# Kernel optimization log

Hardware: AMD Instinct MI355X
Metric: run time of the kernel (lower is better)

## Reference

```python
import jax, jax.numpy as jnp
import numpy as np

N = 100000      # nodes
E = 3200000     # edges (before self-loops)
F_IN = 512      # input feature dim
H1, H2 = 64, 128
C = 40          # num classes
EPS = 1e-5      # BatchNorm eps


def setup_inputs() -> dict:
    key = jax.random.key(0)
    ks = jax.random.split(key, 20)
    inp = {
        "x": jax.random.normal(ks[0], (N, F_IN), jnp.float32),
        "edge_index": jax.random.randint(ks[1], (2, E), 0, N, dtype=jnp.int64),
        # GCNConv weights/biases (glorot-ish scale)
        "W1": jax.random.normal(ks[2], (F_IN, H1), jnp.float32) * (1.0 / np.sqrt(F_IN)),
        "b1": jnp.zeros((H1,), jnp.float32),
        "W2": jax.random.normal(ks[3], (H1, H2), jnp.float32) * (1.0 / np.sqrt(H1)),
        "b2": jnp.zeros((H2,), jnp.float32),
        "W3": jax.random.normal(ks[4], (H2, C), jnp.float32) * (1.0 / np.sqrt(H2)),
        "b3": jnp.zeros((C,), jnp.float32),
        # BatchNorm (eval mode: running stats)
        "g1": 1.0 + 0.1 * jax.random.normal(ks[5], (H1,), jnp.float32),
        "bt1": 0.1 * jax.random.normal(ks[6], (H1,), jnp.float32),
        "rm1": 0.1 * jax.random.normal(ks[7], (H1,), jnp.float32),
        "rv1": jax.random.uniform(ks[8], (H1,), jnp.float32, 0.5, 1.5),
        "g2": 1.0 + 0.1 * jax.random.normal(ks[9], (H2,), jnp.float32),
        "bt2": 0.1 * jax.random.normal(ks[10], (H2,), jnp.float32),
        "rm2": 0.1 * jax.random.normal(ks[11], (H2,), jnp.float32),
        "rv2": jax.random.uniform(ks[12], (H2,), jnp.float32, 0.5, 1.5),
    }
    return inp


def _gcn_norm(edge_index):
    # add self-loops, compute sym-normalized edge weights: d^-1/2[src]*d^-1/2[dst]
    loop = jnp.arange(N, dtype=edge_index.dtype)
    src = jnp.concatenate([edge_index[0], loop])
    dst = jnp.concatenate([edge_index[1], loop])
    deg = jax.ops.segment_sum(jnp.ones_like(dst, jnp.float32), dst, num_segments=N)
    dinv = 1.0 / jnp.sqrt(deg)  # deg >= 1 thanks to self-loops
    norm = dinv[src] * dinv[dst]  # [E+N]
    return src, dst, norm


def _gcn_conv(x, W, b, src, dst, norm):
    h = x @ W                                   # [N, out]
    msg = h[src] * norm[:, None]                # [E+N, out] gather + per-edge scale
    agg = jax.ops.segment_sum(msg, dst, num_segments=N)  # scatter-add
    return agg + b


def _bn_eval(x, gamma, beta, mean, var):
    return (x - mean) * (gamma / jnp.sqrt(var + EPS)) + beta


def reference(x, edge_index, W1, b1, W2, b2, W3, b3,
              g1, bt1, rm1, rv1, g2, bt2, rm2, rv2):
    src, dst, norm = _gcn_norm(edge_index)
    h = jax.nn.relu(_bn_eval(_gcn_conv(x, W1, b1, src, dst, norm), g1, bt1, rm1, rv1))
    # dropout p=0.3: identity in eval mode
    h = jax.nn.relu(_bn_eval(_gcn_conv(h, W2, b2, src, dst, norm), g2, bt2, rm2, rv2))
    h = _gcn_conv(h, W3, b3, src, dst, norm)
    return jax.nn.log_softmax(h, axis=1)
```

## Files before the change

### kernel.cpp

```cpp
#include <hip/hip_runtime.h>
#include <hip/hip_bf16.h>

#define NN 100000
#define FIN 512
#define H1D 64
#define H2D 128
#define CD 40
#define GP 64
#define BNEPS 1e-5f

#define BSHIFT 9
#define BSZ 512
#define NB 196
#define CHUNK 8192

typedef __attribute__((ext_vector_type(8))) short bf16x8;
typedef __attribute__((ext_vector_type(4))) float f32x4;

__device__ __forceinline__ float bf2f(ushort u) {
    union { uint i; float f; } v; v.i = ((uint)u) << 16; return v.f;
}
__device__ __forceinline__ ushort f2bf(float f) {
    union { float f; uint i; } v; v.f = f;
    uint x = v.i;
    return (ushort)((x + 0x7fffu + ((x >> 16) & 1u)) >> 16);
}

__device__ __forceinline__ void acc8(float* a, uint4 v) {
    a[0] += bf2f((ushort)(v.x & 0xffff)); a[1] += bf2f((ushort)(v.x >> 16));
    a[2] += bf2f((ushort)(v.y & 0xffff)); a[3] += bf2f((ushort)(v.y >> 16));
    a[4] += bf2f((ushort)(v.z & 0xffff)); a[5] += bf2f((ushort)(v.z >> 16));
    a[6] += bf2f((ushort)(v.w & 0xffff)); a[7] += bf2f((ushort)(v.w >> 16));
}


__global__ __launch_bounds__(256) void bhist_k(const int* __restrict__ dst, int E,
                                               int* __restrict__ bcount) {
    __shared__ int h[NB];
    for (int i = threadIdx.x; i < NB; i += 256) h[i] = 0;
    __syncthreads();
    int i = blockIdx.x * blockDim.x + threadIdx.x;
    int st = gridDim.x * blockDim.x;
    for (; i < E; i += st) atomicAdd(&h[dst[i] >> BSHIFT], 1);
    __syncthreads();
    for (int j = threadIdx.x; j < NB; j += 256)
        if (h[j]) atomicAdd(&bcount[j], h[j]);
}

__global__ __launch_bounds__(256) void bscan_k(const int* __restrict__ bcount,
                                               int* __restrict__ bstart,
                                               int* __restrict__ bcursor) {
    __shared__ int sh[NB];
    int tid = threadIdx.x;
    if (tid < NB) sh[tid] = bcount[tid];
    __syncthreads();
    for (int off = 1; off < NB; off <<= 1) {
        int v = (tid < NB && tid >= off) ? sh[tid - off] : 0;
        __syncthreads();
        if (tid < NB) sh[tid] += v;
        __syncthreads();
    }
    if (tid < NB) {
        int s = tid ? sh[tid - 1] : 0;
        bstart[tid] = s;
        bcursor[tid] = s;
    }
    if (tid == 0) bstart[NB] = sh[NB - 1];
}

__global__ __launch_bounds__(256) void bscatter_k(const int* __restrict__ src,
                                                  const int* __restrict__ dst, int E,
                                                  int* __restrict__ bcursor,
                                                  int* __restrict__ ebuf) {
    __shared__ int hist[NB];
    __shared__ int loff[NB];
    __shared__ int lcur[NB];
    __shared__ int gbase[NB];
    __shared__ int sbuf[CHUNK];
    int tid = threadIdx.x;
    int e0 = blockIdx.x * CHUNK;
    int e1 = e0 + CHUNK; if (e1 > E) e1 = E;

    for (int i = tid; i < NB; i += 256) hist[i] = 0;
    __syncthreads();
    for (int i = e0 + tid; i < e1; i += 256) atomicAdd(&hist[dst[i] >> BSHIFT], 1);
    __syncthreads();
    int v = (tid < NB) ? hist[tid] : 0;
    __syncthreads();
    if (tid < NB) loff[tid] = v;
    __syncthreads();
    for (int off = 1; off < NB; off <<= 1) {
        int u = (tid < NB && tid >= off) ? loff[tid - off] : 0;
        __syncthreads();
        if (tid < NB) loff[tid] += u;
        __syncthreads();
    }
    if (tid < NB) {
        int excl = loff[tid] - v;
        loff[tid] = excl;
        lcur[tid] = excl;
        gbase[tid] = (v > 0) ? atomicAdd(&bcursor[tid], v) : 0;
    }
    __syncthreads();
    for (int i = e0 + tid; i < e1; i += 256) {
        int d = dst[i];
        int b = d >> BSHIFT;
        int pos = atomicAdd(&lcur[b], 1);
        sbuf[pos] = (src[i] << BSHIFT) | (d & (BSZ - 1));
    }
    __syncthreads();
    int wave = tid >> 6, lane = tid & 63;
    for (int b = wave; b < NB; b += 4) {
        int cnt = (b + 1 < NB ? loff[b + 1] : (e1 - e0)) - loff[b];
        int s0 = loff[b], d0 = gbase[b];
        for (int k = lane; k < cnt; k += 64) ebuf[d0 + k] = sbuf[s0 + k];
    }
}

__global__ __launch_bounds__(256) void bcsr_k(const int* __restrict__ ebuf,
                                              const int* __restrict__ bstart,
                                              int* __restrict__ rowstart,
                                              float* __restrict__ dinv,
                                              int* __restrict__ csr, int E) {
    __shared__ int ldeg[BSZ];
    __shared__ int lcur[BSZ];
    __shared__ int s2[256];
    int b = blockIdx.x, tid = threadIdx.x;
    int node0 = b << BSHIFT;
    int es = bstart[b], ee = bstart[b + 1];
    ldeg[tid] = 0; ldeg[tid + 256] = 0;
    __syncthreads();
    for (int i = es + tid; i < ee; i += 256) atomicAdd(&ldeg[ebuf[i] & (BSZ - 1)], 1);
    __syncthreads();
    int a0 = ldeg[2 * tid], a1 = ldeg[2 * tid + 1];
    s2[tid] = a0 + a1;
    __syncthreads();
    for (int off = 1; off < 256; off <<= 1) {
        int u = (tid >= off) ? s2[tid - off] : 0;
        __syncthreads();
        s2[tid] += u;
        __syncthreads();
    }
    int base2 = tid ? s2[tid - 1] : 0;
    int ex0 = base2, ex1 = base2 + a0;
    int n0 = node0 + 2 * tid, n1 = n0 + 1;
    if (n0 < NN) { rowstart[n0] = es + ex0; dinv[n0] = rsqrtf((float)(a0 + 1)); }
    if (n1 < NN) { rowstart[n1] = es + ex1; dinv[n1] = rsqrtf((float)(a1 + 1)); }
    lcur[2 * tid] = es + ex0;
    lcur[2 * tid + 1] = es + ex1;
    __syncthreads();
    for (int i = es + tid; i < ee; i += 256) {
        int e = ebuf[i];
        int pos = atomicAdd(&lcur[e & (BSZ - 1)], 1);
        csr[pos] = ((unsigned)e) >> BSHIFT;
    }
    if (b == 0 && tid == 0) rowstart[NN] = E;
}

__global__ __launch_bounds__(256) void w1cvt_k(const float* __restrict__ W1,
                                               ushort* __restrict__ w1t) {
    int i = blockIdx.x * 256 + threadIdx.x;
    if (i < FIN * H1D) {
        int n = i >> 9, k = i & 511;
        w1t[i] = f2bf(W1[k * H1D + n]);
    }
}

#define BPAD 520
__global__ __launch_bounds__(256) void gemm1_k(const float* __restrict__ x,
                                               const ushort* __restrict__ w1t,
                                               const float* __restrict__ dinv,
                                               ushort* __restrict__ t1) {
    __shared__ ushort sB[H1D * BPAD];
    int tid = threadIdx.x;
    {
        int row = tid >> 2, seg = tid & 3;
        const uint4* srcp = (const uint4*)(w1t + row * FIN + seg * 128);
        uint4* dstp = (uint4*)(sB + row * BPAD + seg * 128);
#pragma unroll
        for (int j = 0; j < 16; ++j) dstp[j] = srcp[j];
    }
    __syncthreads();
    int wave = tid >> 6, lane = tid & 63;
    int lm = lane & 15, q = lane >> 4;
    int r0 = blockIdx.x * 64 + wave * 16;
    int mrow = r0 + lm;
    int mc = mrow < NN ? mrow : NN - 1;
    const float* ap = x + (size_t)mc * FIN + q * 8;
    const ushort* bp = sB + (size_t)lm * BPAD + q * 8;
    f32x4 acc0 = {0.f, 0.f, 0.f, 0.f}, acc1 = acc0, acc2 = acc0, acc3 = acc0;
#pragma unroll 4
    for (int kb = 0; kb < FIN; kb += 32) {
        float4 a01 = *(const float4*)(ap + kb);
        float4 a23 = *(const float4*)(ap + kb + 4);
        union { bf16x8 v8; __hip_bfloat162 h2[4]; } ua;
        ua.h2[0] = __float22bfloat162_rn(make_float2(a01.x, a01.y));
        ua.h2[1] = __float22bfloat162_rn(make_float2(a01.z, a01.w));
        ua.h2[2] = __float22bfloat162_rn(make_float2(a23.x, a23.y));
        ua.h2[3] = __float22bfloat162_rn(make_float2(a23.z, a23.w));
        bf16x8 b0 = *(const bf16x8*)(bp + kb);
        bf16x8 b1 = *(const bf16x8*)(bp + 16 * BPAD + kb);
        bf16x8 b2 = *(const bf16x8*)(bp + 32 * BPAD + kb);
        bf16x8 b3 = *(const bf16x8*)(bp + 48 * BPAD + kb);
        acc0 = __builtin_amdgcn_mfma_f32_16x16x32_bf16(ua.v8, b0, acc0, 0, 0, 0);
        acc1 = __builtin_amdgcn_mfma_f32_16x16x32_bf16(ua.v8, b1, acc1, 0, 0, 0);
        acc2 = __builtin_amdgcn_mfma_f32_16x16x32_bf16(ua.v8, b2, acc2, 0, 0, 0);
        acc3 = __builtin_amdgcn_mfma_f32_16x16x32_bf16(ua.v8, b3, acc3, 0, 0, 0);
    }
    int rbase = r0 + q * 4;
#pragma unroll
    for (int r = 0; r < 4; ++r) {
        int row = rbase + r;
        if (row < NN) {
            float dv = dinv[row];
            ushort* o = t1 + (size_t)row * H1D;
            o[lm]      = f2bf(acc0[r] * dv);
            o[16 + lm] = f2bf(acc1[r] * dv);
            o[32 + lm] = f2bf(acc2[r] * dv);
            o[48 + lm] = f2bf(acc3[r] * dv);
        }
    }
}

template <int MODE>
__global__ __launch_bounds__(256) void agg64_k(const ushort* __restrict__ tin,
                                               ushort* __restrict__ tout,
                                               const int* __restrict__ rowstart,
                                               const int* __restrict__ csr,
                                               const float* __restrict__ dinv,
                                               const float* __restrict__ g,
                                               const float* __restrict__ bt,
                                               const float* __restrict__ rm,
                                               const float* __restrict__ rv,
                                               const float* __restrict__ b) {
    int wid = (blockIdx.x * blockDim.x + threadIdx.x) >> 6;
    int lane = threadIdx.x & 63;
    if (wid >= NN) return;
    int gsl = lane >> 3;
    int c   = lane & 7;
    int rs = rowstart[wid], re = rowstart[wid + 1];
    float a[8];
#pragma unroll
    for (int j = 0; j < 8; ++j) a[j] = 0.f;
    int i = rs;
    for (; i + 32 <= re; i += 32) {
        int s0 = csr[i + gsl];
        int s1 = csr[i + 8 + gsl];
        int s2 = csr[i + 16 + gsl];
        int s3 = csr[i + 24 + gsl];
        uint4 v0 = *(const uint4*)(tin + (size_t)s0 * H1D + 8 * c);
        uint4 v1 = *(const uint4*)(tin + (size_t)s1 * H1D + 8 * c);
        uint4 v2 = *(const uint4*)(tin + (size_t)s2 * H1D + 8 * c);
        uint4 v3 = *(const uint4*)(tin + (size_t)s3 * H1D + 8 * c);
        acc8(a, v0); acc8(a, v1); acc8(a, v2); acc8(a, v3);
    }
    for (; i + 8 <= re; i += 8) {
        int s0 = csr[i + gsl];
        uint4 v0 = *(const uint4*)(tin + (size_t)s0 * H1D + 8 * c);
        acc8(a, v0);
    }
    if (i + gsl < re) {
        int s0 = csr[i + gsl];
        uint4 v0 = *(const uint4*)(tin + (size_t)s0 * H1D + 8 * c);
        acc8(a, v0);
    }
#pragma unroll
    for (int j = 0; j < 8; ++j) a[j] += __shfl_xor(a[j], 8);
#pragma unroll
    for (int j = 0; j < 8; ++j) a[j] += __shfl_xor(a[j], 16);
#pragma unroll
    for (int j = 0; j < 8; ++j) a[j] += __shfl_xor(a[j], 32);
    {
        uint4 sv = *(const uint4*)(tin + (size_t)wid * H1D + 8 * c);
        acc8(a, sv);
    }
    float dv = dinv[wid];
    float z[8];
    if (MODE == 1) {
        int f0 = 8 * c;
        float4 G0 = *(const float4*)(g + f0),  G1 = *(const float4*)(g + f0 + 4);
        float4 V0 = *(const float4*)(rv + f0), V1 = *(const float4*)(rv + f0 + 4);
        float4 B0 = *(const float4*)(b + f0),  B1 = *(const float4*)(b + f0 + 4);
        float4 M0 = *(const float4*)(rm + f0), M1 = *(const float4*)(rm + f0 + 4);
        float4 T0 = *(const float4*)(bt + f0), T1 = *(const float4*)(bt + f0 + 4);
        float sc[8] = { G0.x * rsqrtf(V0.x + BNEPS), G0.y * rsqrtf(V0.y + BNEPS),
                        G0.z * rsqrtf(V0.z + BNEPS), G0.w * rsqrtf(V0.w + BNEPS),
                        G1.x * rsqrtf(V1.x + BNEPS), G1.y * rsqrtf(V1.y + BNEPS),
                        G1.z * rsqrtf(V1.z + BNEPS), G1.w * rsqrtf(V1.w + BNEPS) };
        float sh[8] = { (B0.x - M0.x) * sc[0] + T0.x, (B0.y - M0.y) * sc[1] + T0.y,
                        (B0.z - M0.z) * sc[2] + T0.z, (B0.w - M0.w) * sc[3] + T0.w,
                        (B1.x - M1.x) * sc[4] + T1.x, (B1.y - M1.y) * sc[5] + T1.y,
                        (B1.z - M1.z) * sc[6] + T1.z, (B1.w - M1.w) * sc[7] + T1.w };
#pragma unroll
        for (int j = 0; j < 8; ++j)
            z[j] = fmaxf(a[j] * dv * sc[j] + sh[j], 0.f) * dv;
    } else {
#pragma unroll
        for (int j = 0; j < 8; ++j) z[j] = a[j] * dv;
    }
    if (gsl == 0) {
        uint4 o;
        o.x = (uint)f2bf(z[0]) | ((uint)f2bf(z[1]) << 16);
        o.y = (uint)f2bf(z[2]) | ((uint)f2bf(z[3]) << 16);
        o.z = (uint)f2bf(z[4]) | ((uint)f2bf(z[5]) << 16);
        o.w = (uint)f2bf(z[6]) | ((uint)f2bf(z[7]) << 16);
        *(uint4*)(tout + (size_t)wid * H1D + 8 * c) = o;
    }
}

__global__ __launch_bounds__(256) void p2p3_k(const ushort* __restrict__ u2,
                                              const float* __restrict__ W2,
                                              const float* __restrict__ b2,
                                              const float* __restrict__ W3,
                                              const float* __restrict__ g2,
                                              const float* __restrict__ bt2,
                                              const float* __restrict__ rm2,
                                              const float* __restrict__ rv2,
                                              const float* __restrict__ dinv,
                                              ushort* __restrict__ g3) {
    __shared__ float sW2[H1D * H2D];
    __shared__ float sW3[H2D * CD];
    __shared__ float sc2[H2D], sh2[H2D];
    int tid = threadIdx.x;
    for (int i = tid; i < H1D * H2D; i += 256) sW2[i] = W2[i];
    for (int i = tid; i < H2D * CD; i += 256) sW3[i] = W3[i];
    if (tid < H2D) {
        float s = g2[tid] * rsqrtf(rv2[tid] + BNEPS);
        sc2[tid] = s;
        sh2[tid] = (b2[tid] - rm2[tid]) * s + bt2[tid];
    }
    __syncthreads();
    int node = blockIdx.x * 256 + tid;
    if (node >= NN) return;
    float u[H1D];
    const uint4* up = (const uint4*)(u2 + (size_t)node * H1D);
#pragma unroll
    for (int i = 0; i < 8; ++i) {
        uint4 v = up[i];
        u[8 * i + 0] = bf2f((ushort)(v.x & 0xffff)); u[8 * i + 1] = bf2f((ushort)(v.x >> 16));
        u[8 * i + 2] = bf2f((ushort)(v.y & 0xffff)); u[8 * i + 3] = bf2f((ushort)(v.y >> 16));
        u[8 * i + 4] = bf2f((ushort)(v.z & 0xffff)); u[8 * i + 5] = bf2f((ushort)(v.z >> 16));
        u[8 * i + 6] = bf2f((ushort)(v.w & 0xffff)); u[8 * i + 7] = bf2f((ushort)(v.w >> 16));
    }
    float gacc[CD];
#pragma unroll
    for (int c = 0; c < CD; ++c) gacc[c] = 0.f;
    for (int fc = 0; fc < H2D; fc += 32) {
        float a[32];
#pragma unroll
        for (int j = 0; j < 32; ++j) a[j] = 0.f;
        for (int l = 0; l < H1D; ++l) {
            float ul = u[l];
            const float4* wr = (const float4*)&sW2[l * H2D + fc];
#pragma unroll
            for (int j = 0; j < 8; ++j) {
                float4 w = wr[j];
                a[4 * j]     += ul * w.x;
                a[4 * j + 1] += ul * w.y;
                a[4 * j + 2] += ul * w.z;
                a[4 * j + 3] += ul * w.w;
            }
        }
#pragma unroll
        for (int j = 0; j < 32; ++j) {
            int f = fc + j;
            float hv = fmaxf(a[j] * sc2[f] + sh2[f], 0.f);
            const float4* w3r = (const float4*)&sW3[f * CD];
#pragma unroll
            for (int c = 0; c < 10; ++c) {
                float4 w = w3r[c];
                gacc[4 * c]     += hv * w.x;
                gacc[4 * c + 1] += hv * w.y;
                gacc[4 * c + 2] += hv * w.z;
                gacc[4 * c + 3] += hv * w.w;
            }
        }
    }
    float dv = dinv[node];
    ushort* op = g3 + (size_t)node * GP;
#pragma unroll
    for (int c = 0; c < 10; ++c) {
        uint pk  = (uint)f2bf(gacc[4 * c] * dv)     | ((uint)f2bf(gacc[4 * c + 1] * dv) << 16);
        uint pk2 = (uint)f2bf(gacc[4 * c + 2] * dv) | ((uint)f2bf(gacc[4 * c + 3] * dv) << 16);
        *(uint2*)&op[4 * c] = make_uint2(pk, pk2);
    }
}

__global__ __launch_bounds__(256) void agg40_k(const ushort* __restrict__ g3,
                                               const float* __restrict__ b3,
                                               const int* __restrict__ rowstart,
                                               const int* __restrict__ csr,
                                               const float* __restrict__ dinv,
                                               float* __restrict__ out) {
    int wid = (blockIdx.x * blockDim.x + threadIdx.x) >> 6;
    int lane = threadIdx.x & 63;
    if (wid >= NN) return;
    int gsl = lane >> 3;
    int c   = lane & 7;
    int rs = rowstart[wid], re = rowstart[wid + 1];
    float a[8];
#pragma unroll
    for (int j = 0; j < 8; ++j) a[j] = 0.f;
    if (c < 5) {
        int i = rs;
        for (; i + 32 <= re; i += 32) {
            int s0 = csr[i + gsl];
            int s1 = csr[i + 8 + gsl];
            int s2 = csr[i + 16 + gsl];
            int s3 = csr[i + 24 + gsl];
            uint4 v0 = *(const uint4*)(g3 + (size_t)s0 * GP + 8 * c);
            uint4 v1 = *(const uint4*)(g3 + (size_t)s1 * GP + 8 * c);
            uint4 v2 = *(const uint4*)(g3 + (size_t)s2 * GP + 8 * c);
            uint4 v3 = *(const uint4*)(g3 + (size_t)s3 * GP + 8 * c);
            acc8(a, v0); acc8(a, v1); acc8(a, v2); acc8(a, v3);
        }
        for (; i + 8 <= re; i += 8) {
            int s0 = csr[i + gsl];
            uint4 v0 = *(const uint4*)(g3 + (size_t)s0 * GP + 8 * c);
            acc8(a, v0);
        }
        if (i + gsl < re) {
            int s0 = csr[i + gsl];
            uint4 v0 = *(const uint4*)(g3 + (size_t)s0 * GP + 8 * c);
            acc8(a, v0);
        }
    }
#pragma unroll
    for (int j = 0; j < 8; ++j) a[j] += __shfl_xor(a[j], 8);
#pragma unroll
    for (int j = 0; j < 8; ++j) a[j] += __shfl_xor(a[j], 16);
#pragma unroll
    for (int j = 0; j < 8; ++j) a[j] += __shfl_xor(a[j], 32);
    if (c < 5) {
        uint4 sv = *(const uint4*)(g3 + (size_t)wid * GP + 8 * c);
        acc8(a, sv);
    }
    float dv = dinv[wid];
    float z[8];
    if (c < 5) {
        int f0 = 8 * c;
        float4 bb0 = *(const float4*)(b3 + f0);
        float4 bb1 = *(const float4*)(b3 + f0 + 4);
        z[0] = a[0] * dv + bb0.x; z[1] = a[1] * dv + bb0.y;
        z[2] = a[2] * dv + bb0.z; z[3] = a[3] * dv + bb0.w;
        z[4] = a[4] * dv + bb1.x; z[5] = a[5] * dv + bb1.y;
        z[6] = a[6] * dv + bb1.z; z[7] = a[7] * dv + bb1.w;
    } else {
#pragma unroll
        for (int j = 0; j < 8; ++j) z[j] = -1e30f;
    }
    float m = fmaxf(fmaxf(fmaxf(z[0], z[1]), fmaxf(z[2], z[3])),
                    fmaxf(fmaxf(z[4], z[5]), fmaxf(z[6], z[7])));
    m = fmaxf(m, __shfl_xor(m, 1));
    m = fmaxf(m, __shfl_xor(m, 2));
    m = fmaxf(m, __shfl_xor(m, 4));
    float e = 0.f;
    if (c < 5) {
#pragma unroll
        for (int j = 0; j < 8; ++j) e += __expf(z[j] - m);
    }
    e += __shfl_xor(e, 1);
    e += __shfl_xor(e, 2);
    e += __shfl_xor(e, 4);
    float ls = __logf(e);
    if (gsl == 0 && c < 5) {
        int f0 = 8 * c;
        float4 o0 = { z[0] - m - ls, z[1] - m - ls, z[2] - m - ls, z[3] - m - ls };
        float4 o1 = { z[4] - m - ls, z[5] - m - ls, z[6] - m - ls, z[7] - m - ls };
        *(float4*)(out + (size_t)wid * CD + f0)     = o0;
        *(float4*)(out + (size_t)wid * CD + f0 + 4) = o1;
    }
}


extern "C" void kernel_launch(void* const* d_in, const int* in_sizes, int n_in,
                              void* d_out, int out_size, void* d_ws, size_t ws_size,
                              hipStream_t stream) {
    (void)n_in; (void)out_size; (void)ws_size;
    const float* x   = (const float*)d_in[0];
    const int*   ei  = (const int*)d_in[1];
    const float* W1  = (const float*)d_in[2];
    const float* b1  = (const float*)d_in[3];
    const float* W2  = (const float*)d_in[4];
    const float* b2  = (const float*)d_in[5];
    const float* W3  = (const float*)d_in[6];
    const float* b3  = (const float*)d_in[7];
    const float* g1  = (const float*)d_in[8];
    const float* bt1 = (const float*)d_in[9];
    const float* rm1 = (const float*)d_in[10];
    const float* rv1 = (const float*)d_in[11];
    const float* g2  = (const float*)d_in[12];
    const float* bt2 = (const float*)d_in[13];
    const float* rm2 = (const float*)d_in[14];
    const float* rv2 = (const float*)d_in[15];
    float* out = (float*)d_out;
    const int E = in_sizes[1] / 2;

    char* w = (char*)d_ws;
    auto alloc = [&](size_t bytes) { char* p = w; w += (bytes + 511) & ~(size_t)511; return p; };
    int*    bcount   = (int*)alloc((size_t)NB * 4);
    int*    bstart   = (int*)alloc((size_t)(NB + 1) * 4);
    int*    bcursor  = (int*)alloc((size_t)NB * 4);
    int*    rowstart = (int*)alloc((size_t)(NN + 1) * 4);
    float*  dinv     = (float*)alloc((size_t)NN * 4);
    int*    csr      = (int*)alloc((size_t)E * 4);
    int*    ebuf     = (int*)alloc((size_t)E * 4);
    ushort* w1t      = (ushort*)alloc((size_t)H1D * FIN * 2);
    ushort* t1       = (ushort*)alloc((size_t)NN * H1D * 2);
    ushort* t2       = (ushort*)alloc((size_t)NN * H1D * 2);
    ushort* g3       = (ushort*)alloc((size_t)NN * GP * 2);

    hipMemsetAsync(bcount, 0, (size_t)NB * 4, stream);
    bhist_k<<<512, 256, 0, stream>>>(ei + E, E, bcount);
    bscan_k<<<1, 256, 0, stream>>>(bcount, bstart, bcursor);
    bscatter_k<<<(E + CHUNK - 1) / CHUNK, 256, 0, stream>>>(ei, ei + E, E, bcursor, ebuf);
    bcsr_k<<<NB, 256, 0, stream>>>(ebuf, bstart, rowstart, dinv, csr, E);
    w1cvt_k<<<(FIN * H1D + 255) / 256, 256, 0, stream>>>(W1, w1t);
    gemm1_k<<<(NN + 63) / 64, 256, 0, stream>>>(x, w1t, dinv, t1);
    agg64_k<1><<<(NN + 3) / 4, 256, 0, stream>>>(t1, t2, rowstart, csr, dinv, g1, bt1, rm1, rv1, b1);
    agg64_k<2><<<(NN + 3) / 4, 256, 0, stream>>>(t2, t1, rowstart, csr, dinv, nullptr, nullptr, nullptr, nullptr, nullptr);
    p2p3_k<<<(NN + 255) / 256, 256, 0, stream>>>(t1, W2, b2, W3, g2, bt2, rm2, rv2, dinv, g3);
    agg40_k<<<(NN + 3) / 4, 256, 0, stream>>>(g3, b3, rowstart, csr, dinv, out);
}
```

Baseline: 734.6 us.

## Process two nodes per wave in aggregation kernels with predicated gathers

Each wave in the three aggregation kernels now handles two consecutive nodes at once. Their neighbor gathers are interleaved in one loop, and the tail is masked with zero-selects rather than branches, so each wave keeps more loads in flight and has fewer serial tail steps. The first GEMM also switches its input x loads to nontemporal loads to reduce cache pollution. The cost is more register pressure, wasted dummy loads when the two nodes' degrees differ, and agg40 now gathers all 8 lanes' columns even where c>=5.

```diff
diff --git a/kernel.cpp b/kernel.cpp
--- a/kernel.cpp
+++ b/kernel.cpp
@@ -31,6 +31,10 @@
     a[2] += bf2f((ushort)(v.y & 0xffff)); a[3] += bf2f((ushort)(v.y >> 16));
     a[4] += bf2f((ushort)(v.z & 0xffff)); a[5] += bf2f((ushort)(v.z >> 16));
     a[6] += bf2f((ushort)(v.w & 0xffff)); a[7] += bf2f((ushort)(v.w >> 16));
+}
+
+__device__ __forceinline__ uint4 selz(bool q, uint4 v) {
+    return q ? v : make_uint4(0u, 0u, 0u, 0u);
 }
 
 
@@ -191,13 +195,13 @@
     f32x4 acc0 = {0.f, 0.f, 0.f, 0.f}, acc1 = acc0, acc2 = acc0, acc3 = acc0;
 #pragma unroll 4
     for (int kb = 0; kb < FIN; kb += 32) {
-        float4 a01 = *(const float4*)(ap + kb);
-        float4 a23 = *(const float4*)(ap + kb + 4);
+        f32x4 a01 = __builtin_nontemporal_load((const f32x4*)(ap + kb));
+        f32x4 a23 = __builtin_nontemporal_load((const f32x4*)(ap + kb + 4));
         union { bf16x8 v8; __hip_bfloat162 h2[4]; } ua;
-        ua.h2[0] = __float22bfloat162_rn(make_float2(a01.x, a01.y));
-        ua.h2[1] = __float22bfloat162_rn(make_float2(a01.z, a01.w));
-        ua.h2[2] = __float22bfloat162_rn(make_float2(a23.x, a23.y));
-        ua.h2[3] = __float22bfloat162_rn(make_float2(a23.z, a23.w));
+        ua.h2[0] = __float22bfloat162_rn(make_float2(a01[0], a01[1]));
+        ua.h2[1] = __float22bfloat162_rn(make_float2(a01[2], a01[3]));
+        ua.h2[2] = __float22bfloat162_rn(make_float2(a23[0], a23[1]));
+        ua.h2[3] = __float22bfloat162_rn(make_float2(a23[2], a23[3]));
         bf16x8 b0 = *(const bf16x8*)(bp + kb);
         bf16x8 b1 = *(const bf16x8*)(bp + 16 * BPAD + kb);
         bf16x8 b2 = *(const bf16x8*)(bp + 32 * BPAD + kb);
@@ -232,52 +236,105 @@
                                                const float* __restrict__ bt,
                                                const float* __restrict__ rm,
                                                const float* __restrict__ rv,
-                                               const float* __restrict__ b) {
-    int wid = (blockIdx.x * blockDim.x + threadIdx.x) >> 6;
+                                               const float* __restrict__ b,
+                                               int E) {
+    int w = (blockIdx.x * blockDim.x + threadIdx.x) >> 6;
     int lane = threadIdx.x & 63;
-    if (wid >= NN) return;
-    int gsl = lane >> 3;
-    int c   = lane & 7;
-    int rs = rowstart[wid], re = rowstart[wid + 1];
-    float a[8];
-#pragma unroll
-    for (int j = 0; j < 8; ++j) a[j] = 0.f;
-    int i = rs;
-    for (; i + 32 <= re; i += 32) {
-        int s0 = csr[i + gsl];
-        int s1 = csr[i + 8 + gsl];
-        int s2 = csr[i + 16 + gsl];
-        int s3 = csr[i + 24 + gsl];
-        uint4 v0 = *(const uint4*)(tin + (size_t)s0 * H1D + 8 * c);
-        uint4 v1 = *(const uint4*)(tin + (size_t)s1 * H1D + 8 * c);
-        uint4 v2 = *(const uint4*)(tin + (size_t)s2 * H1D + 8 * c);
-        uint4 v3 = *(const uint4*)(tin + (size_t)s3 * H1D + 8 * c);
-        acc8(a, v0); acc8(a, v1); acc8(a, v2); acc8(a, v3);
-    }
-    for (; i + 8 <= re; i += 8) {
-        int s0 = csr[i + gsl];
-        uint4 v0 = *(const uint4*)(tin + (size_t)s0 * H1D + 8 * c);
-        acc8(a, v0);
-    }
-    if (i + gsl < re) {
-        int s0 = csr[i + gsl];
-        uint4 v0 = *(const uint4*)(tin + (size_t)s0 * H1D + 8 * c);
-        acc8(a, v0);
-    }
+    int nA = 2 * w;
+    if (nA >= NN) return;
+    int nB = nA + 1;
+    int gsl = lane >> 3, c = lane & 7;
+    int base = 8 * c;
+    int2 r01 = *(const int2*)(rowstart + nA);
+    int reB = rowstart[nA + 2];
+    int iA = r01.x, reA = r01.y;
+    int iB = reA;
+    int Em1 = E - 1;
+    float a[8], y[8];
+#pragma unroll
+    for (int j = 0; j < 8; ++j) { a[j] = 0.f; y[j] = 0.f; }
+
+    for (;;) {
+        bool dA = (iA + 32 <= reA);
+        bool dB = (iB + 32 <= reB);
+        if (!(dA | dB)) break;
+        int jA0 = dA ? iA + gsl      : Em1;
+        int jA1 = dA ? iA + 8 + gsl  : Em1;
+        int jA2 = dA ? iA + 16 + gsl : Em1;
+        int jA3 = dA ? iA + 24 + gsl : Em1;
+        int jB0 = dB ? iB + gsl      : Em1;
+        int jB1 = dB ? iB + 8 + gsl  : Em1;
+        int jB2 = dB ? iB + 16 + gsl : Em1;
+        int jB3 = dB ? iB + 24 + gsl : Em1;
+        int sA0 = csr[jA0], sA1 = csr[jA1], sA2 = csr[jA2], sA3 = csr[jA3];
+        int sB0 = csr[jB0], sB1 = csr[jB1], sB2 = csr[jB2], sB3 = csr[jB3];
+        uint4 vA0 = *(const uint4*)(tin + (size_t)sA0 * H1D + base);
+        uint4 vA1 = *(const uint4*)(tin + (size_t)sA1 * H1D + base);
+        uint4 vA2 = *(const uint4*)(tin + (size_t)sA2 * H1D + base);
+        uint4 vA3 = *(const uint4*)(tin + (size_t)sA3 * H1D + base);
+        uint4 vB0 = *(const uint4*)(tin + (size_t)sB0 * H1D + base);
+        uint4 vB1 = *(const uint4*)(tin + (size_t)sB1 * H1D + base);
+        uint4 vB2 = *(const uint4*)(tin + (size_t)sB2 * H1D + base);
+        uint4 vB3 = *(const uint4*)(tin + (size_t)sB3 * H1D + base);
+        vA0 = selz(dA, vA0); vA1 = selz(dA, vA1); vA2 = selz(dA, vA2); vA3 = selz(dA, vA3);
+        vB0 = selz(dB, vB0); vB1 = selz(dB, vB1); vB2 = selz(dB, vB2); vB3 = selz(dB, vB3);
+        acc8(a, vA0); acc8(a, vA1); acc8(a, vA2); acc8(a, vA3);
+        acc8(y, vB0); acc8(y, vB1); acc8(y, vB2); acc8(y, vB3);
+        iA += dA ? 32 : 0;
+        iB += dB ? 32 : 0;
+    }
+    {
+        bool qA0 = iA + gsl < reA,      qB0 = iB + gsl < reB;
+        bool qA1 = iA + 8 + gsl < reA,  qB1 = iB + 8 + gsl < reB;
+        bool qA2 = iA + 16 + gsl < reA, qB2 = iB + 16 + gsl < reB;
+        bool qA3 = iA + 24 + gsl < reA, qB3 = iB + 24 + gsl < reB;
+        int jA0 = qA0 ? iA + gsl      : Em1;
+        int jA1 = qA1 ? iA + 8 + gsl  : Em1;
+        int jA2 = qA2 ? iA + 16 + gsl : Em1;
+        int jA3 = qA3 ? iA + 24 + gsl : Em1;
+        int jB0 = qB0 ? iB + gsl      : Em1;
+        int jB1 = qB1 ? iB + 8 + gsl  : Em1;
+        int jB2 = qB2 ? iB + 16 + gsl : Em1;
+        int jB3 = qB3 ? iB + 24 + gsl : Em1;
+        int sA0 = csr[jA0], sA1 = csr[jA1], sA2 = csr[jA2], sA3 = csr[jA3];
+        int sB0 = csr[jB0], sB1 = csr[jB1], sB2 = csr[jB2], sB3 = csr[jB3];
+        uint4 vA0 = *(const uint4*)(tin + (size_t)sA0 * H1D + base);
+        uint4 vA1 = *(const uint4*)(tin + (size_t)sA1 * H1D + base);
+        uint4 vA2 = *(const uint4*)(tin + (size_t)sA2 * H1D + base);
+        uint4 vA3 = *(const uint4*)(tin + (size_t)sA3 * H1D + base);
+        uint4 vB0 = *(const uint4*)(tin + (size_t)sB0 * H1D + base);
+        uint4 vB1 = *(const uint4*)(tin + (size_t)sB1 * H1D + base);
+        uint4 vB2 = *(const uint4*)(tin + (size_t)sB2 * H1D + base);
+        uint4 vB3 = *(const uint4*)(tin + (size_t)sB3 * H1D + base);
+        vA0 = selz(qA0, vA0); vA1 = selz(qA1, vA1); vA2 = selz(qA2, vA2); vA3 = selz(qA3, vA3);
+        vB0 = selz(qB0, vB0); vB1 = selz(qB1, vB1); vB2 = selz(qB2, vB2); vB3 = selz(qB3, vB3);
+        acc8(a, vA0); acc8(a, vA1); acc8(a, vA2); acc8(a, vA3);
+        acc8(y, vB0); acc8(y, vB1); acc8(y, vB2); acc8(y, vB3);
+    }
+    uint4 svA = *(const uint4*)(tin + (size_t)nA * H1D + base);
+    uint4 svB = *(const uint4*)(tin + (size_t)nB * H1D + base);
 #pragma unroll
     for (int j = 0; j < 8; ++j) a[j] += __shfl_xor(a[j], 8);
 #pragma unroll
     for (int j = 0; j < 8; ++j) a[j] += __shfl_xor(a[j], 16);
 #pragma unroll
     for (int j = 0; j < 8; ++j) a[j] += __shfl_xor(a[j], 32);
-    {
-        uint4 sv = *(const uint4*)(tin + (size_t)wid * H1D + 8 * c);
-        acc8(a, sv);
-    }
-    float dv = dinv[wid];
+#pragma unroll
+    for (int j = 0; j < 8; ++j) y[j] += __shfl_xor(y[j], 8);
+#pragma unroll
+    for (int j = 0; j < 8; ++j) y[j] += __shfl_xor(y[j], 16);
+#pragma unroll
+    for (int j = 0; j < 8; ++j) y[j] += __shfl_xor(y[j], 32);
+    acc8(a, svA);
+    acc8(y, svB);
+    float2 dv2 = *(const float2*)(dinv + nA);
+    float dv = (gsl == 0) ? dv2.x : dv2.y;
+    float s[8];
+#pragma unroll
+    for (int j = 0; j < 8; ++j) s[j] = (gsl == 0) ? a[j] : y[j];
     float z[8];
     if (MODE == 1) {
-        int f0 = 8 * c;
+        int f0 = base;
         float4 G0 = *(const float4*)(g + f0),  G1 = *(const float4*)(g + f0 + 4);
         float4 V0 = *(const float4*)(rv + f0), V1 = *(const float4*)(rv + f0 + 4);
         float4 B0 = *(const float4*)(b + f0),  B1 = *(const float4*)(b + f0 + 4);
@@ -293,18 +350,18 @@
                         (B1.z - M1.z) * sc[6] + T1.z, (B1.w - M1.w) * sc[7] + T1.w };
 #pragma unroll
         for (int j = 0; j < 8; ++j)
-            z[j] = fmaxf(a[j] * dv * sc[j] + sh[j], 0.f) * dv;
+            z[j] = fmaxf(s[j] * dv * sc[j] + sh[j], 0.f) * dv;
     } else {
 #pragma unroll
-        for (int j = 0; j < 8; ++j) z[j] = a[j] * dv;
-    }
-    if (gsl == 0) {
+        for (int j = 0; j < 8; ++j) z[j] = s[j] * dv;
+    }
+    if (gsl < 2) {
         uint4 o;
         o.x = (uint)f2bf(z[0]) | ((uint)f2bf(z[1]) << 16);
         o.y = (uint)f2bf(z[2]) | ((uint)f2bf(z[3]) << 16);
         o.z = (uint)f2bf(z[4]) | ((uint)f2bf(z[5]) << 16);
         o.w = (uint)f2bf(z[6]) | ((uint)f2bf(z[7]) << 16);
-        *(uint4*)(tout + (size_t)wid * H1D + 8 * c) = o;
+        *(uint4*)(tout + (size_t)(nA + gsl) * H1D + base) = o;
     }
 }
 
@@ -391,60 +448,110 @@
                                                const int* __restrict__ rowstart,
                                                const int* __restrict__ csr,
                                                const float* __restrict__ dinv,
-                                               float* __restrict__ out) {
-    int wid = (blockIdx.x * blockDim.x + threadIdx.x) >> 6;
+                                               float* __restrict__ out,
+                                               int E) {
+    int w = (blockIdx.x * blockDim.x + threadIdx.x) >> 6;
     int lane = threadIdx.x & 63;
-    if (wid >= NN) return;
-    int gsl = lane >> 3;
-    int c   = lane & 7;
-    int rs = rowstart[wid], re = rowstart[wid + 1];
-    float a[8];
-#pragma unroll
-    for (int j = 0; j < 8; ++j) a[j] = 0.f;
-    if (c < 5) {
-        int i = rs;
-        for (; i + 32 <= re; i += 32) {
-            int s0 = csr[i + gsl];
-            int s1 = csr[i + 8 + gsl];
-            int s2 = csr[i + 16 + gsl];
-            int s3 = csr[i + 24 + gsl];
-            uint4 v0 = *(const uint4*)(g3 + (size_t)s0 * GP + 8 * c);
-            uint4 v1 = *(const uint4*)(g3 + (size_t)s1 * GP + 8 * c);
-            uint4 v2 = *(const uint4*)(g3 + (size_t)s2 * GP + 8 * c);
-            uint4 v3 = *(const uint4*)(g3 + (size_t)s3 * GP + 8 * c);
-            acc8(a, v0); acc8(a, v1); acc8(a, v2); acc8(a, v3);
-        }
-        for (; i + 8 <= re; i += 8) {
-            int s0 = csr[i + gsl];
-            uint4 v0 = *(const uint4*)(g3 + (size_t)s0 * GP + 8 * c);
-            acc8(a, v0);
-        }
-        if (i + gsl < re) {
-            int s0 = csr[i + gsl];
-            uint4 v0 = *(const uint4*)(g3 + (size_t)s0 * GP + 8 * c);
-            acc8(a, v0);
-        }
-    }
+    int nA = 2 * w;
+    if (nA >= NN) return;
+    int nB = nA + 1;
+    int gsl = lane >> 3, c = lane & 7;
+    int base = 8 * c;
+    int2 r01 = *(const int2*)(rowstart + nA);
+    int reB = rowstart[nA + 2];
+    int iA = r01.x, reA = r01.y;
+    int iB = reA;
+    int Em1 = E - 1;
+    float a[8], y[8];
+#pragma unroll
+    for (int j = 0; j < 8; ++j) { a[j] = 0.f; y[j] = 0.f; }
+
+    for (;;) {
+        bool dA = (iA + 32 <= reA);
+        bool dB = (iB + 32 <= reB);
+        if (!(dA | dB)) break;
+        int jA0 = dA ? iA + gsl      : Em1;
+        int jA1 = dA ? iA + 8 + gsl  : Em1;
+        int jA2 = dA ? iA + 16 + gsl : Em1;
+        int jA3 = dA ? iA + 24 + gsl : Em1;
+        int jB0 = dB ? iB + gsl      : Em1;
+        int jB1 = dB ? iB + 8 + gsl  : Em1;
+        int jB2 = dB ? iB + 16 + gsl : Em1;
+        int jB3 = dB ? iB + 24 + gsl : Em1;
+        int sA0 = csr[jA0], sA1 = csr[jA1], sA2 = csr[jA2], sA3 = csr[jA3];
+        int sB0 = csr[jB0], sB1 = csr[jB1], sB2 = csr[jB2], sB3 = csr[jB3];
+        uint4 vA0 = *(const uint4*)(g3 + (size_t)sA0 * GP + base);
+        uint4 vA1 = *(const uint4*)(g3 + (size_t)sA1 * GP + base);
+        uint4 vA2 = *(const uint4*)(g3 + (size_t)sA2 * GP + base);
+        uint4 vA3 = *(const uint4*)(g3 + (size_t)sA3 * GP + base);
+        uint4 vB0 = *(const uint4*)(g3 + (size_t)sB0 * GP + base);
+        uint4 vB1 = *(const uint4*)(g3 + (size_t)sB1 * GP + base);
+        uint4 vB2 = *(const uint4*)(g3 + (size_t)sB2 * GP + base);
+        uint4 vB3 = *(const uint4*)(g3 + (size_t)sB3 * GP + base);
+        vA0 = selz(dA, vA0); vA1 = selz(dA, vA1); vA2 = selz(dA, vA2); vA3 = selz(dA, vA3);
+        vB0 = selz(dB, vB0); vB1 = selz(dB, vB1); vB2 = selz(dB, vB2); vB3 = selz(dB, vB3);
+        acc8(a, vA0); acc8(a, vA1); acc8(a, vA2); acc8(a, vA3);
+        acc8(y, vB0); acc8(y, vB1); acc8(y, vB2); acc8(y, vB3);
+        iA += dA ? 32 : 0;
+        iB += dB ? 32 : 0;
+    }
+    {
+        bool qA0 = iA + gsl < reA,      qB0 = iB + gsl < reB;
+        bool qA1 = iA + 8 + gsl < reA,  qB1 = iB + 8 + gsl < reB;
+        bool qA2 = iA + 16 + gsl < reA, qB2 = iB + 16 + gsl < reB;
+        bool qA3 = iA + 24 + gsl < reA, qB3 = iB + 24 + gsl < reB;
+        int jA0 = qA0 ? iA + gsl      : Em1;
+        int jA1 = qA1 ? iA + 8 + gsl  : Em1;
+        int jA2 = qA2 ? iA + 16 + gsl : Em1;
+        int jA3 = qA3 ? iA + 24 + gsl : Em1;
+        int jB0 = qB0 ? iB + gsl      : Em1;
+        int jB1 = qB1 ? iB + 8 + gsl  : Em1;
+        int jB2 = qB2 ? iB + 16 + gsl : Em1;
+        int jB3 = qB3 ? iB + 24 + gsl : Em1;
+        int sA0 = csr[jA0], sA1 = csr[jA1], sA2 = csr[jA2], sA3 = csr[jA3];
+        int sB0 = csr[jB0], sB1 = csr[jB1], sB2 = csr[jB2], sB3 = csr[jB3];
+        uint4 vA0 = *(const uint4*)(g3 + (size_t)sA0 * GP + base);
+        uint4 vA1 = *(const uint4*)(g3 + (size_t)sA1 * GP + base);
+        uint4 vA2 = *(const uint4*)(g3 + (size_t)sA2 * GP + base);
+        uint4 vA3 = *(const uint4*)(g3 + (size_t)sA3 * GP + base);
+        uint4 vB0 = *(const uint4*)(g3 + (size_t)sB0 * GP + base);
+        uint4 vB1 = *(const uint4*)(g3 + (size_t)sB1 * GP + base);
+        uint4 vB2 = *(const uint4*)(g3 + (size_t)sB2 * GP + base);
+        uint4 vB3 = *(const uint4*)(g3 + (size_t)sB3 * GP + base);
+        vA0 = selz(qA0, vA0); vA1 = selz(qA1, vA1); vA2 = selz(qA2, vA2); vA3 = selz(qA3, vA3);
+        vB0 = selz(qB0, vB0); vB1 = selz(qB1, vB1); vB2 = selz(qB2, vB2); vB3 = selz(qB3, vB3);
+        acc8(a, vA0); acc8(a, vA1); acc8(a, vA2); acc8(a, vA3);
+        acc8(y, vB0); acc8(y, vB1); acc8(y, vB2); acc8(y, vB3);
+    }
+    uint4 svA = *(const uint4*)(g3 + (size_t)nA * GP + base);
+    uint4 svB = *(const uint4*)(g3 + (size_t)nB * GP + base);
 #pragma unroll
     for (int j = 0; j < 8; ++j) a[j] += __shfl_xor(a[j], 8);
 #pragma unroll
     for (int j = 0; j < 8; ++j) a[j] += __shfl_xor(a[j], 16);
 #pragma unroll
     for (int j = 0; j < 8; ++j) a[j] += __shfl_xor(a[j], 32);
-    if (c < 5) {
-        uint4 sv = *(const uint4*)(g3 + (size_t)wid * GP + 8 * c);
-        acc8(a, sv);
-    }
-    float dv = dinv[wid];
+#pragma unroll
+    for (int j = 0; j < 8; ++j) y[j] += __shfl_xor(y[j], 8);
+#pragma unroll
+    for (int j = 0; j < 8; ++j) y[j] += __shfl_xor(y[j], 16);
+#pragma unroll
+    for (int j = 0; j < 8; ++j) y[j] += __shfl_xor(y[j], 32);
+    acc8(a, svA);
+    acc8(y, svB);
+    float2 dv2 = *(const float2*)(dinv + nA);
+    float dv = (gsl == 0) ? dv2.x : dv2.y;
+    float s[8];
+#pragma unroll
+    for (int j = 0; j < 8; ++j) s[j] = (gsl == 0) ? a[j] : y[j];
     float z[8];
     if (c < 5) {
-        int f0 = 8 * c;
-        float4 bb0 = *(const float4*)(b3 + f0);
-        float4 bb1 = *(const float4*)(b3 + f0 + 4);
-        z[0] = a[0] * dv + bb0.x; z[1] = a[1] * dv + bb0.y;
-        z[2] = a[2] * dv + bb0.z; z[3] = a[3] * dv + bb0.w;
-        z[4] = a[4] * dv + bb1.x; z[5] = a[5] * dv + bb1.y;
-        z[6] = a[6] * dv + bb1.z; z[7] = a[7] * dv + bb1.w;
+        float4 bb0 = *(const float4*)(b3 + base);
+        float4 bb1 = *(const float4*)(b3 + base + 4);
+        z[0] = s[0] * dv + bb0.x; z[1] = s[1] * dv + bb0.y;
+        z[2] = s[2] * dv + bb0.z; z[3] = s[3] * dv + bb0.w;
+        z[4] = s[4] * dv + bb1.x; z[5] = s[5] * dv + bb1.y;
+        z[6] = s[6] * dv + bb1.z; z[7] = s[7] * dv + bb1.w;
     } else {
 #pragma unroll
         for (int j = 0; j < 8; ++j) z[j] = -1e30f;
@@ -463,12 +570,12 @@
     e += __shfl_xor(e, 2);
     e += __shfl_xor(e, 4);
     float ls = __logf(e);
-    if (gsl == 0 && c < 5) {
-        int f0 = 8 * c;
+    if (gsl < 2 && c < 5) {
         float4 o0 = { z[0] - m - ls, z[1] - m - ls, z[2] - m - ls, z[3] - m - ls };
         float4 o1 = { z[4] - m - ls, z[5] - m - ls, z[6] - m - ls, z[7] - m - ls };
-        *(float4*)(out + (size_t)wid * CD + f0)     = o0;
-        *(float4*)(out + (size_t)wid * CD + f0 + 4) = o1;
+        float* orow = out + (size_t)(nA + gsl) * CD + base;
+        *(float4*)(orow)     = o0;
+        *(float4*)(orow + 4) = o1;
     }
 }
 
@@ -510,6 +617,8 @@
     ushort* t2       = (ushort*)alloc((size_t)NN * H1D * 2);
     ushort* g3       = (ushort*)alloc((size_t)NN * GP * 2);
 
+    const int aggblocks = ((NN / 2) + 3) / 4;
+
     hipMemsetAsync(bcount, 0, (size_t)NB * 4, stream);
     bhist_k<<<512, 256, 0, stream>>>(ei + E, E, bcount);
     bscan_k<<<1, 256, 0, stream>>>(bcount, bstart, bcursor);
@@ -517,8 +626,8 @@
     bcsr_k<<<NB, 256, 0, stream>>>(ebuf, bstart, rowstart, dinv, csr, E);
     w1cvt_k<<<(FIN * H1D + 255) / 256, 256, 0, stream>>>(W1, w1t);
     gemm1_k<<<(NN + 63) / 64, 256, 0, stream>>>(x, w1t, dinv, t1);
-    agg64_k<1><<<(NN + 3) / 4, 256, 0, stream>>>(t1, t2, rowstart, csr, dinv, g1, bt1, rm1, rv1, b1);
-    agg64_k<2><<<(NN + 3) / 4, 256, 0, stream>>>(t2, t1, rowstart, csr, dinv, nullptr, nullptr, nullptr, nullptr, nullptr);
+    agg64_k<1><<<aggblocks, 256, 0, stream>>>(t1, t2, rowstart, csr, dinv, g1, bt1, rm1, rv1, b1, E);
+    agg64_k<2><<<aggblocks, 256, 0, stream>>>(t2, t1, rowstart, csr, dinv, nullptr, nullptr, nullptr, nullptr, nullptr, E);
     p2p3_k<<<(NN + 255) / 256, 256, 0, stream>>>(t1, W2, b2, W3, g2, bt2, rm2, rv2, dinv, g3);
-    agg40_k<<<(NN + 3) / 4, 256, 0, stream>>>(g3, b3, rowstart, csr, dinv, out);
-}
+    agg40_k<<<aggblocks, 256, 0, stream>>>(g3, b3, rowstart, csr, dinv, out, E);
+}
```

New measurement: 714.0 us. 2.8% less time.
